# Kernel optimization log

Measured on AMD Instinct MI355X. Metric: run time of the kernel, lower is better.

The kernel has to match this reference:

```python
import jax, jax.numpy as jnp
import numpy as np

VOCAB = 256
BATCH = 524288
WORD_LEN = 16

# 7-d cross product structure constants (Fano plane triples, 1-indexed e_i)
_TRIPLES = [(1, 2, 3), (1, 4, 5), (1, 7, 6), (2, 4, 6), (2, 5, 7), (3, 4, 7), (3, 6, 5)]

def _build_C():
    C = np.zeros((7, 7, 7), dtype=np.float32)
    for (i, j, k) in _TRIPLES:
        i, j, k = i - 1, j - 1, k - 1
        # cyclic permutations +1, anti-cyclic -1
        for (a, b, c) in ((i, j, k), (j, k, i), (k, i, j)):
            C[a, b, c] = 1.0
        for (a, b, c) in ((j, i, k), (i, k, j), (k, j, i)):
            C[a, b, c] = -1.0
    return jnp.asarray(C)

_C = _build_C()

def _cross7(a, b):
    # a, b: (..., 7) -> (..., 7)
    return jnp.einsum('ijk,...i,...j->...k', _C, a, b)

def setup_inputs() -> dict:
    key = jax.random.key(0)
    k_ids, k_emb = jax.random.split(key)
    input_ids = jax.random.randint(k_ids, (BATCH, WORD_LEN), 0, VOCAB, dtype=jnp.int32)
    embedding = jax.random.normal(k_emb, (VOCAB, 8), dtype=jnp.float32)
    return {"input_ids": input_ids, "embedding": embedding}

def reference(input_ids, embedding):
    oct_emb = embedding[input_ids]          # (B, L, 8)
    imag = oct_emb[..., 1:]                 # (B, L, 7)
    init = imag[:, 0, :]                    # (B, 7)
    rest = jnp.swapaxes(imag[:, 1:, :], 0, 1)  # (L-1, B, 7)

    def step(v, x):
        return _cross7(v, x), None

    word_emb, _ = jax.lax.scan(step, init, rest)
    return word_emb                          # (B, 7)
```

## Files before the change

kernel.cpp:

```cpp
#include <hip/hip_runtime.h>

#define WORD_LEN 16
#define BLOCK 256

__global__ __launch_bounds__(BLOCK, 8) void oct_word_emb_kernel(
    const int* __restrict__ ids,
    const float* __restrict__ emb,
    float* __restrict__ out)
{
    __shared__ float4 slo[256];
    __shared__ float4 shi[256];
    __shared__ float sout[BLOCK * 7];

    const int tid = threadIdx.x;

    {
        const float4* e4 = reinterpret_cast<const float4*>(emb);
        float4 lo = e4[tid * 2 + 0];
        float4 hi = e4[tid * 2 + 1];
        slo[tid] = make_float4(lo.y, lo.z, lo.w, hi.x);
        shi[tid] = make_float4(hi.y, hi.z, hi.w, 0.0f);
    }
    __syncthreads();

    const long long b = (long long)blockIdx.x * BLOCK + tid;

    const int4* id4 = reinterpret_cast<const int4*>(ids + b * WORD_LEN);
    const int4 w0 = id4[0], w1 = id4[1], w2 = id4[2], w3 = id4[3];
    const int id[16] = {w0.x, w0.y, w0.z, w0.w,  w1.x, w1.y, w1.z, w1.w,
                        w2.x, w2.y, w2.z, w2.w,  w3.x, w3.y, w3.z, w3.w};

    float v[7];
    {
        const float4 a = slo[id[0]];
        const float4 h = shi[id[0]];
        v[0] = a.x; v[1] = a.y; v[2] = a.z; v[3] = a.w;
        v[4] = h.x; v[5] = h.y; v[6] = h.z;
    }

    #pragma unroll
    for (int t = 1; t < WORD_LEN; ++t) {
        const float4 a = slo[id[t]];
        const float4 h = shi[id[t]];
        const float x[7] = {a.x, a.y, a.z, a.w, h.x, h.y, h.z};

        float r[7] = {0.f, 0.f, 0.f, 0.f, 0.f, 0.f, 0.f};
        constexpr int TRI[7][3] = {{0,1,2},{0,3,4},{0,6,5},{1,3,5},{1,4,6},{2,3,6},{2,5,4}};
        #pragma unroll
        for (int q = 0; q < 7; ++q) {
            const int i = TRI[q][0], j = TRI[q][1], k = TRI[q][2];
            r[k] = fmaf(v[i], x[j], r[k]);  r[k] = fmaf(-v[j], x[i], r[k]);
            r[i] = fmaf(v[j], x[k], r[i]);  r[i] = fmaf(-v[k], x[j], r[i]);
            r[j] = fmaf(v[k], x[i], r[j]);  r[j] = fmaf(-v[i], x[k], r[j]);
        }
        #pragma unroll
        for (int c = 0; c < 7; ++c) v[c] = r[c];
    }

    {
        float* d = &sout[tid * 7];
        #pragma unroll
        for (int c = 0; c < 7; ++c) d[c] = v[c];
    }
    __syncthreads();

    {
        const float4* so4 = reinterpret_cast<const float4*>(sout);
        float4* o4 = reinterpret_cast<float4*>(out + (size_t)blockIdx.x * BLOCK * 7);
        o4[tid] = so4[tid];
        if (tid < 192) o4[256 + tid] = so4[256 + tid];
    }
}

extern "C" void kernel_launch(void* const* d_in, const int* in_sizes, int n_in,
                              void* d_out, int out_size, void* d_ws, size_t ws_size,
                              hipStream_t stream) {
    const int* ids = (const int*)d_in[0];
    const float* emb = (const float*)d_in[1];
    float* out = (float*)d_out;

    const int batch = in_sizes[0] / WORD_LEN;
    const int grid = batch / BLOCK;

    oct_word_emb_kernel<<<grid, BLOCK, 0, stream>>>(ids, emb, out);
}
```

Before: 17.44 us.

## Coalesce id loads via shared memory with byte packing; write outputs directly

Token ids are now read block-cooperatively with fully coalesced int4 loads, packed into bytes and staged in shared memory. Each thread then reads its 16 packed ids with a single 16-byte LDS load, instead of four strided int4 global loads per thread. The shared-memory staging of outputs is dropped in favour of direct per-thread scalar stores of 7 floats, which are strided and less coalesced. Packing assumes ids fit in 8 bits, which holds because the vocabulary has 256 entries.

```diff
diff --git a/kernel.cpp b/kernel.cpp
--- a/kernel.cpp
+++ b/kernel.cpp
@@ -10,7 +10,7 @@
 {
     __shared__ float4 slo[256];
     __shared__ float4 shi[256];
-    __shared__ float sout[BLOCK * 7];
+    __shared__ __align__(16) unsigned int sids[BLOCK * 4];
 
     const int tid = threadIdx.x;
 
@@ -21,27 +21,35 @@
         slo[tid] = make_float4(lo.y, lo.z, lo.w, hi.x);
         shi[tid] = make_float4(hi.y, hi.z, hi.w, 0.0f);
     }
+
+    {
+        const int4* g = reinterpret_cast<const int4*>(ids) + (size_t)blockIdx.x * (BLOCK * 4);
+        #pragma unroll
+        for (int j = 0; j < 4; ++j) {
+            int4 w = g[j * BLOCK + tid];
+            sids[j * BLOCK + tid] = (unsigned)w.x | ((unsigned)w.y << 8) |
+                                    ((unsigned)w.z << 16) | ((unsigned)w.w << 24);
+        }
+    }
     __syncthreads();
 
-    const long long b = (long long)blockIdx.x * BLOCK + tid;
-
-    const int4* id4 = reinterpret_cast<const int4*>(ids + b * WORD_LEN);
-    const int4 w0 = id4[0], w1 = id4[1], w2 = id4[2], w3 = id4[3];
-    const int id[16] = {w0.x, w0.y, w0.z, w0.w,  w1.x, w1.y, w1.z, w1.w,
-                        w2.x, w2.y, w2.z, w2.w,  w3.x, w3.y, w3.z, w3.w};
+    const uint4 pid = reinterpret_cast<const uint4*>(sids)[tid];
+    const unsigned pw[4] = {pid.x, pid.y, pid.z, pid.w};
 
     float v[7];
     {
-        const float4 a = slo[id[0]];
-        const float4 h = shi[id[0]];
+        const unsigned id0 = pw[0] & 0xff;
+        const float4 a = slo[id0];
+        const float4 h = shi[id0];
         v[0] = a.x; v[1] = a.y; v[2] = a.z; v[3] = a.w;
         v[4] = h.x; v[5] = h.y; v[6] = h.z;
     }
 
     #pragma unroll
     for (int t = 1; t < WORD_LEN; ++t) {
-        const float4 a = slo[id[t]];
-        const float4 h = shi[id[t]];
+        const unsigned idt = (pw[t >> 2] >> ((t & 3) * 8)) & 0xff;
+        const float4 a = slo[idt];
+        const float4 h = shi[idt];
         const float x[7] = {a.x, a.y, a.z, a.w, h.x, h.y, h.z};
 
         float r[7] = {0.f, 0.f, 0.f, 0.f, 0.f, 0.f, 0.f};
@@ -57,19 +65,9 @@
         for (int c = 0; c < 7; ++c) v[c] = r[c];
     }
 
-    {
-        float* d = &sout[tid * 7];
-        #pragma unroll
-        for (int c = 0; c < 7; ++c) d[c] = v[c];
-    }
-    __syncthreads();
-
-    {
-        const float4* so4 = reinterpret_cast<const float4*>(sout);
-        float4* o4 = reinterpret_cast<float4*>(out + (size_t)blockIdx.x * BLOCK * 7);
-        o4[tid] = so4[tid];
-        if (tid < 192) o4[256 + tid] = so4[256 + tid];
-    }
+    float* o = out + ((size_t)blockIdx.x * BLOCK + tid) * 7;
+    #pragma unroll
+    for (int c = 0; c < 7; ++c) o[c] = v[c];
 }
 
 extern "C" void kernel_launch(void* const* d_in, const int* in_sizes, int n_in,
```

Measured after the change: 17.93 us. 2.8% more time.

## Process two words per thread and write outputs directly to global memory

Applied to the files above, without the earlier changes.

Each thread now handles two words, halving the grid and the per-block shared-memory table load, and issues both words' id loads up front for more memory-level parallelism. The cross-product is rewritten as explicit scalar FMA chains. The shared-memory staging of outputs is dropped in favour of direct strided scalar global stores. This may reduce store coalescing, and the occupancy hint is lowered.

```diff
diff --git a/kernel.cpp b/kernel.cpp
--- a/kernel.cpp
+++ b/kernel.cpp
@@ -2,18 +2,61 @@
 
 #define WORD_LEN 16
 #define BLOCK 256
+#define WPT 2
 
-__global__ __launch_bounds__(BLOCK, 8) void oct_word_emb_kernel(
+__device__ __forceinline__ void process_word(
+    const float4* __restrict__ slo, const float4* __restrict__ shi,
+    int4 w0, int4 w1, int4 w2, int4 w3, float* __restrict__ o)
+{
+    const int id[16] = {w0.x, w0.y, w0.z, w0.w,  w1.x, w1.y, w1.z, w1.w,
+                        w2.x, w2.y, w2.z, w2.w,  w3.x, w3.y, w3.z, w3.w};
+
+    float v0, v1, v2, v3, v4, v5, v6;
+    {
+        const float4 a = slo[id[0]];
+        const float4 h = shi[id[0]];
+        v0 = a.x; v1 = a.y; v2 = a.z; v3 = a.w;
+        v4 = h.x; v5 = h.y; v6 = h.z;
+    }
+
+    #pragma unroll
+    for (int t = 1; t < WORD_LEN; ++t) {
+        const float4 a = shi ? slo[id[t]] : a;
+        const float4 aa = slo[id[t]];
+        const float4 hh = shi[id[t]];
+        const float x0 = aa.x, x1 = aa.y, x2 = aa.z, x3 = aa.w;
+        const float x4 = hh.x, x5 = hh.y, x6 = hh.z;
+
+        float r0 = v1 * x2;  r0 = fmaf(-v2, x1, r0);  r0 = fmaf(v3, x4, r0);
+        r0 = fmaf(-v4, x3, r0);  r0 = fmaf(v6, x5, r0);  r0 = fmaf(-v5, x6, r0);
+        float r1 = v2 * x0;  r1 = fmaf(-v0, x2, r1);  r1 = fmaf(v3, x5, r1);
+        r1 = fmaf(-v5, x3, r1);  r1 = fmaf(v4, x6, r1);  r1 = fmaf(-v6, x4, r1);
+        float r2 = v0 * x1;  r2 = fmaf(-v1, x0, r2);  r2 = fmaf(v3, x6, r2);
+        r2 = fmaf(-v6, x3, r2);  r2 = fmaf(v5, x4, r2);  r2 = fmaf(-v4, x5, r2);
+        float r3 = v4 * x0;  r3 = fmaf(-v0, x4, r3);  r3 = fmaf(v5, x1, r3);
+        r3 = fmaf(-v1, x5, r3);  r3 = fmaf(v6, x2, r3);  r3 = fmaf(-v2, x6, r3);
+        float r4 = v0 * x3;  r4 = fmaf(-v3, x0, r4);  r4 = fmaf(v6, x1, r4);
+        r4 = fmaf(-v1, x6, r4);  r4 = fmaf(v2, x5, r4);  r4 = fmaf(-v5, x2, r4);
+        float r5 = v0 * x6;  r5 = fmaf(-v6, x0, r5);  r5 = fmaf(v1, x3, r5);
+        r5 = fmaf(-v3, x1, r5);  r5 = fmaf(v4, x2, r5);  r5 = fmaf(-v2, x4, r5);
+        float r6 = v5 * x0;  r6 = fmaf(-v0, x5, r6);  r6 = fmaf(v1, x4, r6);
+        r6 = fmaf(-v4, x1, r6);  r6 = fmaf(v2, x3, r6);  r6 = fmaf(-v3, x2, r6);
+
+        v0 = r0; v1 = r1; v2 = r2; v3 = r3; v4 = r4; v5 = r5; v6 = r6;
+    }
+
+    o[0] = v0; o[1] = v1; o[2] = v2; o[3] = v3; o[4] = v4; o[5] = v5; o[6] = v6;
+}
+
+__global__ __launch_bounds__(BLOCK, 4) void oct_word_emb_kernel(
     const int* __restrict__ ids,
     const float* __restrict__ emb,
     float* __restrict__ out)
 {
     __shared__ float4 slo[256];
     __shared__ float4 shi[256];
-    __shared__ float sout[BLOCK * 7];
 
     const int tid = threadIdx.x;
-
     {
         const float4* e4 = reinterpret_cast<const float4*>(emb);
         float4 lo = e4[tid * 2 + 0];
@@ -23,53 +66,17 @@
     }
     __syncthreads();
 
-    const long long b = (long long)blockIdx.x * BLOCK + tid;
+    const size_t wbase = (size_t)blockIdx.x * (BLOCK * WPT);
+    const size_t wa = wbase + tid;
+    const size_t wb = wbase + BLOCK + tid;
 
-    const int4* id4 = reinterpret_cast<const int4*>(ids + b * WORD_LEN);
-    const int4 w0 = id4[0], w1 = id4[1], w2 = id4[2], w3 = id4[3];
-    const int id[16] = {w0.x, w0.y, w0.z, w0.w,  w1.x, w1.y, w1.z, w1.w,
-                        w2.x, w2.y, w2.z, w2.w,  w3.x, w3.y, w3.z, w3.w};
+    const int4* ga = reinterpret_cast<const int4*>(ids) + wa * 4;
+    const int4* gb = reinterpret_cast<const int4*>(ids) + wb * 4;
+    const int4 a0 = ga[0], a1 = ga[1], a2 = ga[2], a3 = ga[3];
+    const int4 b0 = gb[0], b1 = gb[1], b2 = gb[2], b3 = gb[3];
 
-    float v[7];
-    {
-        const float4 a = slo[id[0]];
-        const float4 h = shi[id[0]];
-        v[0] = a.x; v[1] = a.y; v[2] = a.z; v[3] = a.w;
-        v[4] = h.x; v[5] = h.y; v[6] = h.z;
-    }
-
-    #pragma unroll
-    for (int t = 1; t < WORD_LEN; ++t) {
-        const float4 a = slo[id[t]];
-        const float4 h = shi[id[t]];
-        const float x[7] = {a.x, a.y, a.z, a.w, h.x, h.y, h.z};
-
-        float r[7] = {0.f, 0.f, 0.f, 0.f, 0.f, 0.f, 0.f};
-        constexpr int TRI[7][3] = {{0,1,2},{0,3,4},{0,6,5},{1,3,5},{1,4,6},{2,3,6},{2,5,4}};
-        #pragma unroll
-        for (int q = 0; q < 7; ++q) {
-            const int i = TRI[q][0], j = TRI[q][1], k = TRI[q][2];
-            r[k] = fmaf(v[i], x[j], r[k]);  r[k] = fmaf(-v[j], x[i], r[k]);
-            r[i] = fmaf(v[j], x[k], r[i]);  r[i] = fmaf(-v[k], x[j], r[i]);
-            r[j] = fmaf(v[k], x[i], r[j]);  r[j] = fmaf(-v[i], x[k], r[j]);
-        }
-        #pragma unroll
-        for (int c = 0; c < 7; ++c) v[c] = r[c];
-    }
-
-    {
-        float* d = &sout[tid * 7];
-        #pragma unroll
-        for (int c = 0; c < 7; ++c) d[c] = v[c];
-    }
-    __syncthreads();
-
-    {
-        const float4* so4 = reinterpret_cast<const float4*>(sout);
-        float4* o4 = reinterpret_cast<float4*>(out + (size_t)blockIdx.x * BLOCK * 7);
-        o4[tid] = so4[tid];
-        if (tid < 192) o4[256 + tid] = so4[256 + tid];
-    }
+    process_word(slo, shi, a0, a1, a2, a3, out + wa * 7);
+    process_word(slo, shi, b0, b1, b2, b3, out + wb * 7);
 }
 
 extern "C" void kernel_launch(void* const* d_in, const int* in_sizes, int n_in,
@@ -80,7 +87,7 @@
     float* out = (float*)d_out;
 
     const int batch = in_sizes[0] / WORD_LEN;
-    const int grid = batch / BLOCK;
+    const int grid = batch / (BLOCK * WPT);
 
     oct_word_emb_kernel<<<grid, BLOCK, 0, stream>>>(ids, emb, out);
 }
```

Result: slower. 17.98 us (+3.1%).
